# Optimization experiments

Hardware: AMD Instinct MI355X
Metric: run time of the kernel (lower is better)

## Reference

```python
import jax, jax.numpy as jnp
import numpy as np
from jax import lax

VOL, PATCH, DIM, DEPTH, HEADS, DIM_HEAD, MLP, CH, B = 64, 8, 768, 4, 12, 64, 3072, 1, 2
INNER = HEADS * DIM_HEAD
GS = VOL // PATCH              # 8 -> N = 512 tokens
EPS = 1e-5


def _sincos_1d(embed_dim, pos):
    omega = np.arange(embed_dim // 2, dtype=float) / (embed_dim / 2.0)
    omega = 1.0 / 10000 ** omega
    out = np.einsum('m,d->md', pos.reshape(-1), omega)
    return np.concatenate([np.sin(out), np.cos(out)], axis=1)


def _pos_embed_3d(embed_dim, gs):
    gd = np.arange(gs, dtype=np.float32)
    gh = np.arange(gs, dtype=np.float32)
    gw = np.arange(gs, dtype=np.float32)
    grid = np.stack(np.meshgrid(gw, gh, gd), axis=0).reshape([3, 1, gs, gs, gs])
    emb = np.concatenate([_sincos_1d(embed_dim // 3, grid[i]) for i in range(3)], axis=1)
    return jnp.asarray(emb, jnp.float32)[None]  # [1, N, dim]


def setup_inputs() -> dict:
    key = jax.random.key(0)
    ks = jax.random.split(key, 12)
    s = 0.02  # xavier-like small init scale
    d = {
        'volume': jax.random.normal(ks[0], (B, CH, VOL, VOL, VOL), jnp.float32),
        'conv_w': jax.random.normal(ks[1], (DIM, CH, PATCH, PATCH, PATCH), jnp.float32) * s,
        'conv_b': jnp.zeros((DIM,), jnp.float32),
        'pos_embed': _pos_embed_3d(DIM, GS),
        'ln1_w': jnp.ones((DEPTH, DIM), jnp.float32),
        'ln1_b': jnp.zeros((DEPTH, DIM), jnp.float32),
        'w_qkv': jax.random.normal(ks[2], (DEPTH, DIM, 3 * INNER), jnp.float32) * s,
        'w_o': jax.random.normal(ks[3], (DEPTH, INNER, DIM), jnp.float32) * s,
        'b_o': jnp.zeros((DEPTH, DIM), jnp.float32),
        'ln2_w': jnp.ones((DEPTH, DIM), jnp.float32),
        'ln2_b': jnp.zeros((DEPTH, DIM), jnp.float32),
        'w1': jax.random.normal(ks[4], (DEPTH, DIM, MLP), jnp.float32) * s,
        'b1': jnp.zeros((DEPTH, MLP), jnp.float32),
        'w2': jax.random.normal(ks[5], (DEPTH, MLP, DIM), jnp.float32) * s,
        'b2': jnp.zeros((DEPTH, DIM), jnp.float32),
        'lnf_w': jnp.ones((DIM,), jnp.float32),
        'lnf_b': jnp.zeros((DIM,), jnp.float32),
    }
    return d


def _ln(x, w, b):
    m = jnp.mean(x, axis=-1, keepdims=True)
    v = jnp.mean(jnp.square(x - m), axis=-1, keepdims=True)
    return (x - m) * lax.rsqrt(v + EPS) * w + b


def _forward(volume, conv_w, conv_b, pos_embed, ln1_w, ln1_b, w_qkv, w_o, b_o,
             ln2_w, ln2_b, w1, b1, w2, b2, lnf_w, lnf_b):
    # Conv3d patch embedding (stride == kernel == patch)
    x = lax.conv_general_dilated(volume, conv_w, window_strides=(PATCH,) * 3,
                                 padding='VALID',
                                 dimension_numbers=('NCDHW', 'OIDHW', 'NCDHW'))
    x = x + conv_b[None, :, None, None, None]
    b = x.shape[0]
    x = x.reshape(b, DIM, -1).transpose(0, 2, 1)   # b (d h w) c -> [B, N, dim]
    x = x + pos_embed
    scale = DIM_HEAD ** -0.5

    def layer(x, p):
        l1w, l1b, wqkv, wo, bo, l2w, l2b, W1, B1, W2, B2 = p
        h = _ln(x, l1w, l1b)
        qkv = h @ wqkv                               # [B, N, 3*inner]
        q, k, v = jnp.split(qkv, 3, axis=-1)
        def heads(t):
            bsz, n, _ = t.shape
            return t.reshape(bsz, n, HEADS, DIM_HEAD).transpose(0, 2, 1, 3)
        q, k, v = heads(q), heads(k), heads(v)
        attn = jax.nn.softmax(jnp.einsum('bhqd,bhkd->bhqk', q, k) * scale, axis=-1)
        o = jnp.einsum('bhqk,bhkd->bhqd', attn, v)   # [B, H, N, dh]
        o = o.transpose(0, 2, 1, 3).reshape(x.shape[0], -1, INNER)
        x = x + (o @ wo + bo)
        h = _ln(x, l2w, l2b)
        x = x + (jnp.tanh(h @ W1 + B1) @ W2 + B2)
        return x, None

    params = (ln1_w, ln1_b, w_qkv, w_o, b_o, ln2_w, ln2_b, w1, b1, w2, b2)
    x, _ = lax.scan(layer, x, params)
    return _ln(x, lnf_w, lnf_b)


def reference(volume, conv_w, conv_b, pos_embed, ln1_w, ln1_b, w_qkv, w_o, b_o,
              ln2_w, ln2_b, w1, b1, w2, b2, lnf_w, lnf_b):
    return _forward(volume, conv_w, conv_b, pos_embed, ln1_w, ln1_b, w_qkv, w_o, b_o,
                    ln2_w, ln2_b, w1, b1, w2, b2, lnf_w, lnf_b)
```

## Files before the change

### kernel.cpp

```cpp
#include <hip/hip_runtime.h>
#include <hip/hip_bf16.h>

typedef __hip_bfloat16 bf16;
typedef short bf16x8 __attribute__((ext_vector_type(8)));
typedef float f32x4 __attribute__((ext_vector_type(4)));

__device__ __forceinline__ float b2f(bf16 v) { return __bfloat162float(v); }
__device__ __forceinline__ void storev(float* p, float v) { *p = v; }
__device__ __forceinline__ void storev(bf16* p, float v) { *p = __float2bfloat16(v); }

__device__ __forceinline__ void gl2lds16(const bf16* g, bf16* l) {
  __builtin_amdgcn_global_load_lds(
      (const __attribute__((address_space(1))) unsigned int*)g,
      (__attribute__((address_space(3))) unsigned int*)l, 16, 0, 0);
}

__global__ void im2col_kernel(const float* __restrict__ vol, bf16* __restrict__ out) {
  int t = blockIdx.x;
  int b = t >> 9, n = t & 511;
  int pd = n >> 6, ph = (n >> 3) & 7, pw = n & 7;
  const float* vb = vol + ((size_t)b << 18);
  for (int l = threadIdx.x; l < 512; l += 256) {
    int i = l >> 6, j = (l >> 3) & 7, k = l & 7;
    out[(size_t)t * 512 + l] =
        __float2bfloat16(vb[(pd * 8 + i) * 4096 + (ph * 8 + j) * 64 + (pw * 8 + k)]);
  }
}

__global__ void convert_kernel(const float* __restrict__ in, bf16* __restrict__ out, int n) {
  int i = (blockIdx.x * 256 + threadIdx.x) * 4;
  if (i + 3 < n) {
    float4 v = *(const float4*)&in[i];
    out[i + 0] = __float2bfloat16(v.x);
    out[i + 1] = __float2bfloat16(v.y);
    out[i + 2] = __float2bfloat16(v.z);
    out[i + 3] = __float2bfloat16(v.w);
  }
}

__global__ __launch_bounds__(256) void transpose_all(
    const float* __restrict__ wqkv, const float* __restrict__ wo,
    const float* __restrict__ w1, const float* __restrict__ w2,
    bf16* __restrict__ tqkv, bf16* __restrict__ two,
    bf16* __restrict__ t1, bf16* __restrict__ t2) {
  int bid = blockIdx.x;
  size_t L = blockIdx.y;
  const float* in;
  bf16* out;
  int R, C, tc, t0;
  if (bid < 432)       { in = wqkv + L * 768 * 2304; out = tqkv + L * 768 * 2304; R = 768;  C = 2304; tc = 36; t0 = bid; }
  else if (bid < 576)  { in = wo + L * 768 * 768;    out = two + L * 768 * 768;   R = 768;  C = 768;  tc = 12; t0 = bid - 432; }
  else if (bid < 1152) { in = w1 + L * 768 * 3072;   out = t1 + L * 768 * 3072;   R = 768;  C = 3072; tc = 48; t0 = bid - 576; }
  else                 { in = w2 + L * 3072 * 768;   out = t2 + L * 3072 * 768;   R = 3072; C = 768;  tc = 12; t0 = bid - 1152; }
  int r0 = (t0 / tc) * 64, c0 = (t0 % tc) * 64;
  __shared__ bf16 Ts[64 * 68];
  int t = threadIdx.x;
  int r = t >> 4, cq = t & 15;
#pragma unroll
  for (int yy = 0; yy < 4; ++yy) {
    int row = r + yy * 16;
    float4 v = *(const float4*)&in[(size_t)(r0 + row) * C + c0 + cq * 4];
    bf16 pk[4] = {__float2bfloat16(v.x), __float2bfloat16(v.y),
                  __float2bfloat16(v.z), __float2bfloat16(v.w)};
    *(uint2*)&Ts[row * 68 + cq * 4] = *(uint2*)pk;
  }
  __syncthreads();
  int oc = t >> 2, seg = t & 3;
  bf16 pk[16];
#pragma unroll
  for (int j = 0; j < 16; ++j) {
    int e = (j + seg * 4) & 15;
    pk[e] = Ts[(seg * 16 + e) * 68 + oc];
  }
  *(uint4*)&out[(size_t)(c0 + oc) * R + r0 + seg * 16] = *(uint4*)&pk[0];
  *(uint4*)&out[(size_t)(c0 + oc) * R + r0 + seg * 16 + 8] = *(uint4*)&pk[8];
}

template <typename OutT>
__global__ __launch_bounds__(256) void ln_kernel(const float* __restrict__ x,
                                                 const float* __restrict__ w,
                                                 const float* __restrict__ b,
                                                 OutT* __restrict__ out) {
  int row = blockIdx.x * 4 + (threadIdx.x >> 6);
  int lane = threadIdx.x & 63;
  const float* xr = x + (size_t)row * 768;
  float v[12];
  float s = 0.f, ss = 0.f;
#pragma unroll
  for (int i = 0; i < 12; ++i) {
    v[i] = xr[lane + i * 64];
    s += v[i];
    ss += v[i] * v[i];
  }
  for (int off = 32; off; off >>= 1) {
    s += __shfl_xor(s, off);
    ss += __shfl_xor(ss, off);
  }
  float m = s * (1.f / 768.f);
  float var = ss * (1.f / 768.f) - m * m;
  float rr = rsqrtf(var + 1e-5f);
#pragma unroll
  for (int i = 0; i < 12; ++i)
    storev(out + (size_t)row * 768 + lane + i * 64,
           (v[i] - m) * rr * w[lane + i * 64] + b[lane + i * 64]);
}

template <int BM, int BN, int EPI>
__global__ __launch_bounds__(256) void mfma_gemm(
    const bf16* __restrict__ A, const bf16* __restrict__ Bt,
    const float* __restrict__ bias, const float* __restrict__ aux,
    bf16* __restrict__ vt,
    void* __restrict__ Cout, int M, int N, int K) {
  constexpr int WTM = BM / 2, WTN = BN / 2;
  constexpr int MT = WTM / 16, NT = WTN / 16;
  __shared__ bf16 As[BM * 64];
  __shared__ bf16 Bs[BN * 64];
  int tid = threadIdx.x;
  int wave = tid >> 6, lane = tid & 63;
  int wm = wave >> 1, wn = wave & 1;
  int m15 = lane & 15, q = lane >> 4;
  int m0 = blockIdx.y * BM, n0 = blockIdx.x * BN;
  int kspan = K / gridDim.z;
  int kbeg = blockIdx.z * kspan, kend = kbeg + kspan;

  f32x4 acc[MT][NT];
#pragma unroll
  for (int i = 0; i < MT; ++i)
#pragma unroll
    for (int j = 0; j < NT; ++j) acc[i][j] = (f32x4){0.f, 0.f, 0.f, 0.f};

  for (int k0 = kbeg; k0 < kend; k0 += 64) {
#pragma unroll
    for (int it = 0; it < BM * 8 / 256; ++it) {
      int c = tid + it * 256;
      int row = c >> 3, cc = c & 7;
      gl2lds16(&A[(size_t)(m0 + row) * K + k0 + cc * 8], &As[c * 8]);
    }
#pragma unroll
    for (int it = 0; it < BN * 8 / 256; ++it) {
      int c = tid + it * 256;
      int row = c >> 3, cc = c & 7;
      gl2lds16(&Bt[(size_t)(n0 + row) * K + k0 + cc * 8], &Bs[c * 8]);
    }
    __syncthreads();
#pragma unroll
    for (int s = 0; s < 2; ++s) {
      bf16x8 af[MT], bfr[NT];
#pragma unroll
      for (int i = 0; i < MT; ++i)
        af[i] = *(const bf16x8*)&As[(wm * WTM + i * 16 + m15) * 64 + s * 32 + q * 8];
#pragma unroll
      for (int j = 0; j < NT; ++j)
        bfr[j] = *(const bf16x8*)&Bs[(wn * WTN + j * 16 + m15) * 64 + s * 32 + q * 8];
#pragma unroll
      for (int i = 0; i < MT; ++i)
#pragma unroll
        for (int j = 0; j < NT; ++j)
          acc[i][j] = __builtin_amdgcn_mfma_f32_16x16x32_bf16(af[i], bfr[j], acc[i][j], 0, 0, 0);
    }
    __syncthreads();
  }

#pragma unroll
  for (int i = 0; i < MT; ++i) {
#pragma unroll
    for (int j = 0; j < NT; ++j) {
      int col = n0 + wn * WTN + j * 16 + m15;
      if (EPI == 4) {
        if (col < 1536) {
#pragma unroll
          for (int r = 0; r < 4; ++r) {
            int row = m0 + wm * WTM + i * 16 + q * 4 + r;
            ((bf16*)Cout)[(size_t)row * 1536 + col] = __float2bfloat16(acc[i][j][r]);
          }
        } else {
          int row0 = m0 + wm * WTM + i * 16 + q * 4;
          int cl = col - 1536;
          int hh = cl >> 6, dd = cl & 63;
          int bb = row0 >> 9, tok = row0 & 511;
          bf16 pk[4];
#pragma unroll
          for (int r = 0; r < 4; ++r) pk[r] = __float2bfloat16(acc[i][j][r]);
          *(uint2*)&vt[((size_t)(bb * 12 + hh) * 64 + dd) * 512 + tok] = *(uint2*)pk;
        }
      } else if (EPI == 5) {
        float bv = (blockIdx.z == 0) ? bias[col] : 0.f;
#pragma unroll
        for (int r = 0; r < 4; ++r) {
          int row = m0 + wm * WTM + i * 16 + q * 4 + r;
          unsafeAtomicAdd(&((float*)Cout)[(size_t)row * N + col], acc[i][j][r] + bv);
        }
      } else {
        float bv = (EPI == 0) ? 0.f : bias[col];
#pragma unroll
        for (int r = 0; r < 4; ++r) {
          int row = m0 + wm * WTM + i * 16 + q * 4 + r;
          float v = acc[i][j][r] + bv;
          if (EPI == 2) v = tanhf(v);
          if (EPI == 3) v += aux[(size_t)(row & 511) * N + col];
          if (EPI == 0 || EPI == 2)
            ((bf16*)Cout)[(size_t)row * N + col] = __float2bfloat16(v);
          else
            ((float*)Cout)[(size_t)row * N + col] = v;
        }
      }
    }
  }
}

__global__ __launch_bounds__(128) void attn_mfma(const bf16* __restrict__ qk,
                                                 const bf16* __restrict__ Vt,
                                                 bf16* __restrict__ o) {
  constexpr int PS = 520;
  __shared__ bf16 KVs[64 * 64];
  __shared__ bf16 P[32 * PS];
  int bh = blockIdx.x;
  int b = bh / 12, hh = bh % 12;
  int q0 = blockIdx.y * 32;
  int tid = threadIdx.x;
  int wave = tid >> 6, lane = tid & 63;
  int n15 = lane & 15, quad = lane >> 4;
  const bf16* qkb = qk + (size_t)b * 512 * 1536;
  int ql = wave * 16 + n15;

  const bf16* qp = qkb + (size_t)(q0 + ql) * 1536 + hh * 64 + quad * 8;
  bf16x8 qf0 = *(const bf16x8*)qp;
  bf16x8 qf1 = *(const bf16x8*)(qp + 32);

  f32x4 S[32];
#pragma unroll
  for (int i = 0; i < 32; ++i) S[i] = (f32x4){0.f, 0.f, 0.f, 0.f};

  const bf16* kbase = qkb + 768 + hh * 64;
#pragma unroll
  for (int kc = 0; kc < 8; ++kc) {
    __syncthreads();
#pragma unroll
    for (int it = 0; it < 4; ++it) {
      int c = tid + it * 128;
      int r = c >> 3, cc = c & 7;
      gl2lds16(&kbase[(size_t)(kc * 64 + r) * 1536 + cc * 8], &KVs[c * 8]);
    }
    __syncthreads();
#pragma unroll
    for (int t = 0; t < 4; ++t) {
      int idx = kc * 4 + t;
      bf16x8 a0 = *(const bf16x8*)&KVs[(t * 16 + n15) * 64 + quad * 8];
      bf16x8 a1 = *(const bf16x8*)&KVs[(t * 16 + n15) * 64 + 32 + quad * 8];
      S[idx] = __builtin_amdgcn_mfma_f32_16x16x32_bf16(a0, qf0, S[idx], 0, 0, 0);
      S[idx] = __builtin_amdgcn_mfma_f32_16x16x32_bf16(a1, qf1, S[idx], 0, 0, 0);
    }
  }

  float mx = -1e30f;
#pragma unroll
  for (int i = 0; i < 32; ++i)
#pragma unroll
    for (int r = 0; r < 4; ++r) { S[i][r] *= 0.125f; mx = fmaxf(mx, S[i][r]); }
  mx = fmaxf(mx, __shfl_xor(mx, 16));
  mx = fmaxf(mx, __shfl_xor(mx, 32));
  float sum = 0.f;
#pragma unroll
  for (int i = 0; i < 32; ++i)
#pragma unroll
    for (int r = 0; r < 4; ++r) { float e = __expf(S[i][r] - mx); S[i][r] = e; sum += e; }
  sum += __shfl_xor(sum, 16);
  sum += __shfl_xor(sum, 32);
  float inv = 1.f / sum;

#pragma unroll
  for (int i = 0; i < 32; ++i) {
    bf16 pk[4];
#pragma unroll
    for (int r = 0; r < 4; ++r) pk[r] = __float2bfloat16(S[i][r] * inv);
    *(uint2*)&P[(size_t)ql * PS + i * 16 + quad * 4] = *(uint2*)pk;
  }

  f32x4 oacc[4];
#pragma unroll
  for (int dt = 0; dt < 4; ++dt) oacc[dt] = (f32x4){0.f, 0.f, 0.f, 0.f};
  const bf16* vtb = Vt + (size_t)bh * 64 * 512;
  for (int kc = 0; kc < 8; ++kc) {
    __syncthreads();
#pragma unroll
    for (int it = 0; it < 4; ++it) {
      int c = tid + it * 128;
      int r = c >> 3, cc = c & 7;
      gl2lds16(&vtb[(size_t)r * 512 + kc * 64 + cc * 8], &KVs[c * 8]);
    }
    __syncthreads();
    bf16x8 p0 = *(const bf16x8*)&P[(size_t)ql * PS + kc * 64 + quad * 8];
    bf16x8 p1 = *(const bf16x8*)&P[(size_t)ql * PS + kc * 64 + 32 + quad * 8];
#pragma unroll
    for (int dt = 0; dt < 4; ++dt) {
      bf16x8 v0 = *(const bf16x8*)&KVs[(dt * 16 + n15) * 64 + quad * 8];
      bf16x8 v1 = *(const bf16x8*)&KVs[(dt * 16 + n15) * 64 + 32 + quad * 8];
      oacc[dt] = __builtin_amdgcn_mfma_f32_16x16x32_bf16(p0, v0, oacc[dt], 0, 0, 0);
      oacc[dt] = __builtin_amdgcn_mfma_f32_16x16x32_bf16(p1, v1, oacc[dt], 0, 0, 0);
    }
  }

#pragma unroll
  for (int dt = 0; dt < 4; ++dt)
#pragma unroll
    for (int r = 0; r < 4; ++r) {
      int tok = q0 + wave * 16 + quad * 4 + r;
      o[((size_t)b * 512 + tok) * 768 + hh * 64 + dt * 16 + n15] =
          __float2bfloat16(oacc[dt][r]);
    }
}

extern "C" void kernel_launch(void* const* d_in, const int* in_sizes, int n_in,
                              void* d_out, int out_size, void* d_ws, size_t ws_size,
                              hipStream_t stream) {
  const float* volume = (const float*)d_in[0];
  const float* conv_w = (const float*)d_in[1];
  const float* conv_b = (const float*)d_in[2];
  const float* pos    = (const float*)d_in[3];
  const float* ln1w   = (const float*)d_in[4];
  const float* ln1b   = (const float*)d_in[5];
  const float* wqkv   = (const float*)d_in[6];
  const float* wo     = (const float*)d_in[7];
  const float* bo     = (const float*)d_in[8];
  const float* ln2w   = (const float*)d_in[9];
  const float* ln2b   = (const float*)d_in[10];
  const float* w1     = (const float*)d_in[11];
  const float* b1     = (const float*)d_in[12];
  const float* w2     = (const float*)d_in[13];
  const float* b2     = (const float*)d_in[14];
  const float* lnfw   = (const float*)d_in[15];
  const float* lnfb   = (const float*)d_in[16];

  char* w = (char*)d_ws;
  float* x    = (float*)(w + 0);
  bf16* h     = (bf16*)(w + 3145728);
  bf16* qk    = (bf16*)(w + 4718592);
  bf16* patchA= qk;
  bf16* Vt    = (bf16*)(w + 7864320);
  bf16* oact  = (bf16*)(w + 9437184);
  bf16* cwb   = (bf16*)(w + 15728640);
  bf16* tqkv  = (bf16*)(w + 16515072);
  bf16* two   = (bf16*)(w + 30670848);
  bf16* t1    = (bf16*)(w + 35389440);
  bf16* t2    = (bf16*)(w + 54263808);

  convert_kernel<<<384, 256, 0, stream>>>(conv_w, cwb, 768 * 512);
  im2col_kernel<<<1024, 256, 0, stream>>>(volume, patchA);
  transpose_all<<<dim3(1728, 4), 256, 0, stream>>>(wqkv, wo, w1, w2, tqkv, two, t1, t2);
  mfma_gemm<64, 64, 3><<<dim3(12, 16), 256, 0, stream>>>(
      patchA, cwb, conv_b, pos, nullptr, x, 1024, 768, 512);

  for (int L = 0; L < 4; ++L) {
    ln_kernel<bf16><<<256, 256, 0, stream>>>(x, ln1w + L * 768, ln1b + L * 768, h);
    mfma_gemm<128, 64, 4><<<dim3(36, 8), 256, 0, stream>>>(
        h, tqkv + (size_t)L * 768 * 2304, nullptr, nullptr, Vt, qk, 1024, 2304, 768);
    attn_mfma<<<dim3(24, 16), 128, 0, stream>>>(qk, Vt, oact);
    mfma_gemm<64, 64, 5><<<dim3(12, 16, 2), 256, 0, stream>>>(
        oact, two + (size_t)L * 768 * 768, bo + L * 768, nullptr, nullptr, x, 1024, 768, 768);
    ln_kernel<bf16><<<256, 256, 0, stream>>>(x, ln2w + L * 768, ln2b + L * 768, h);
    mfma_gemm<128, 64, 2><<<dim3(48, 8), 256, 0, stream>>>(
        h, t1 + (size_t)L * 768 * 3072, b1 + L * 3072, nullptr, nullptr, oact, 1024, 3072, 768);
    mfma_gemm<64, 64, 5><<<dim3(12, 16, 4), 256, 0, stream>>>(
        oact, t2 + (size_t)L * 768 * 3072, b2 + L * 768, nullptr, nullptr, x, 1024, 768, 3072);
  }

  ln_kernel<float><<<256, 256, 0, stream>>>(x, lnfw, lnfb, (float*)d_out);
}
```

Before: 556.0 us.

## Split-K FC1 and patch GEMMs with atomics, shrink QKV tiles, rewrite transpose

FC1 now uses split-K (z=2) with atomic float accumulation into a zeroed fp32 buffer, followed by a separate bias+tanh kernel that writes bf16. The patch-embed GEMM also becomes split-K with atomics after a memset. The QKV GEMM switches to 64x64 tiles to launch more blocks. The weight-transpose kernel is rewritten to use an fp32 shared tile. The goal is more parallelism on a large GPU, paid for with memsets, atomic traffic, an extra fp32 round trip and an additional kernel launch.

```diff
diff --git a/kernel.cpp b/kernel.cpp
--- a/kernel.cpp
+++ b/kernel.cpp
@@ -53,27 +53,27 @@
   else if (bid < 1152) { in = w1 + L * 768 * 3072;   out = t1 + L * 768 * 3072;   R = 768;  C = 3072; tc = 48; t0 = bid - 576; }
   else                 { in = w2 + L * 3072 * 768;   out = t2 + L * 3072 * 768;   R = 3072; C = 768;  tc = 12; t0 = bid - 1152; }
   int r0 = (t0 / tc) * 64, c0 = (t0 % tc) * 64;
-  __shared__ bf16 Ts[64 * 68];
-  int t = threadIdx.x;
-  int r = t >> 4, cq = t & 15;
+  __shared__ float tile[64][65];
+  int tx = threadIdx.x & 15, ty = threadIdx.x >> 4;
 #pragma unroll
   for (int yy = 0; yy < 4; ++yy) {
-    int row = r + yy * 16;
-    float4 v = *(const float4*)&in[(size_t)(r0 + row) * C + c0 + cq * 4];
-    bf16 pk[4] = {__float2bfloat16(v.x), __float2bfloat16(v.y),
-                  __float2bfloat16(v.z), __float2bfloat16(v.w)};
-    *(uint2*)&Ts[row * 68 + cq * 4] = *(uint2*)pk;
+    float4 v = *(const float4*)&in[(size_t)(r0 + ty + yy * 16) * C + c0 + tx * 4];
+    tile[ty + yy * 16][tx * 4 + 0] = v.x;
+    tile[ty + yy * 16][tx * 4 + 1] = v.y;
+    tile[ty + yy * 16][tx * 4 + 2] = v.z;
+    tile[ty + yy * 16][tx * 4 + 3] = v.w;
   }
   __syncthreads();
-  int oc = t >> 2, seg = t & 3;
-  bf16 pk[16];
-#pragma unroll
-  for (int j = 0; j < 16; ++j) {
-    int e = (j + seg * 4) & 15;
-    pk[e] = Ts[(seg * 16 + e) * 68 + oc];
-  }
-  *(uint4*)&out[(size_t)(c0 + oc) * R + r0 + seg * 16] = *(uint4*)&pk[0];
-  *(uint4*)&out[(size_t)(c0 + oc) * R + r0 + seg * 16 + 8] = *(uint4*)&pk[8];
+  int cl = threadIdx.x >> 3;
+  int rb = (threadIdx.x & 7) * 8;
+#pragma unroll
+  for (int half = 0; half < 2; ++half) {
+    int c = cl + half * 32;
+    bf16 pk[8];
+#pragma unroll
+    for (int e = 0; e < 8; ++e) pk[e] = __float2bfloat16(tile[rb + e][c]);
+    *(uint4*)&out[(size_t)(c0 + c) * R + r0 + rb] = *(uint4*)pk;
+  }
 }
 
 template <typename OutT>
@@ -103,6 +103,25 @@
   for (int i = 0; i < 12; ++i)
     storev(out + (size_t)row * 768 + lane + i * 64,
            (v[i] - m) * rr * w[lane + i * 64] + b[lane + i * 64]);
+}
+
+__global__ __launch_bounds__(256) void act_kernel(const float* __restrict__ in,
+                                                  const float* __restrict__ b1,
+                                                  bf16* __restrict__ out) {
+  int row = blockIdx.x, tid = threadIdx.x;
+  const float* ir = in + (size_t)row * 3072;
+  bf16* orow = out + (size_t)row * 3072;
+#pragma unroll
+  for (int i = 0; i < 3; ++i) {
+    int c = tid * 4 + i * 1024;
+    float4 v = *(const float4*)&ir[c];
+    float4 bb = *(const float4*)&b1[c];
+    bf16 pk[4] = {__float2bfloat16(tanhf(v.x + bb.x)),
+                  __float2bfloat16(tanhf(v.y + bb.y)),
+                  __float2bfloat16(tanhf(v.z + bb.z)),
+                  __float2bfloat16(tanhf(v.w + bb.w))};
+    *(uint2*)&orow[c] = *(uint2*)pk;
+  }
 }
 
 template <int BM, int BN, int EPI>
@@ -190,6 +209,20 @@
           int row = m0 + wm * WTM + i * 16 + q * 4 + r;
           unsafeAtomicAdd(&((float*)Cout)[(size_t)row * N + col], acc[i][j][r] + bv);
         }
+      } else if (EPI == 6) {
+#pragma unroll
+        for (int r = 0; r < 4; ++r) {
+          int row = m0 + wm * WTM + i * 16 + q * 4 + r;
+          unsafeAtomicAdd(&((float*)Cout)[(size_t)row * N + col], acc[i][j][r]);
+        }
+      } else if (EPI == 7) {
+#pragma unroll
+        for (int r = 0; r < 4; ++r) {
+          int row = m0 + wm * WTM + i * 16 + q * 4 + r;
+          float v = acc[i][j][r];
+          if (blockIdx.z == 0) v += bias[col] + aux[(size_t)(row & 511) * N + col];
+          unsafeAtomicAdd(&((float*)Cout)[(size_t)row * N + col], v);
+        }
       } else {
         float bv = (EPI == 0) ? 0.f : bias[col];
 #pragma unroll
@@ -197,11 +230,7 @@
           int row = m0 + wm * WTM + i * 16 + q * 4 + r;
           float v = acc[i][j][r] + bv;
           if (EPI == 2) v = tanhf(v);
-          if (EPI == 3) v += aux[(size_t)(row & 511) * N + col];
-          if (EPI == 0 || EPI == 2)
-            ((bf16*)Cout)[(size_t)row * N + col] = __float2bfloat16(v);
-          else
-            ((float*)Cout)[(size_t)row * N + col] = v;
+          ((bf16*)Cout)[(size_t)row * N + col] = __float2bfloat16(v);
         }
       }
     }
@@ -343,23 +372,27 @@
   bf16* two   = (bf16*)(w + 30670848);
   bf16* t1    = (bf16*)(w + 35389440);
   bf16* t2    = (bf16*)(w + 54263808);
+  float* oactf= (float*)(w + 73138176);
 
   convert_kernel<<<384, 256, 0, stream>>>(conv_w, cwb, 768 * 512);
   im2col_kernel<<<1024, 256, 0, stream>>>(volume, patchA);
   transpose_all<<<dim3(1728, 4), 256, 0, stream>>>(wqkv, wo, w1, w2, tqkv, two, t1, t2);
-  mfma_gemm<64, 64, 3><<<dim3(12, 16), 256, 0, stream>>>(
+  hipMemsetAsync(x, 0, 1024 * 768 * sizeof(float), stream);
+  mfma_gemm<64, 64, 7><<<dim3(12, 16, 2), 256, 0, stream>>>(
       patchA, cwb, conv_b, pos, nullptr, x, 1024, 768, 512);
 
   for (int L = 0; L < 4; ++L) {
     ln_kernel<bf16><<<256, 256, 0, stream>>>(x, ln1w + L * 768, ln1b + L * 768, h);
-    mfma_gemm<128, 64, 4><<<dim3(36, 8), 256, 0, stream>>>(
+    mfma_gemm<64, 64, 4><<<dim3(36, 16), 256, 0, stream>>>(
         h, tqkv + (size_t)L * 768 * 2304, nullptr, nullptr, Vt, qk, 1024, 2304, 768);
     attn_mfma<<<dim3(24, 16), 128, 0, stream>>>(qk, Vt, oact);
     mfma_gemm<64, 64, 5><<<dim3(12, 16, 2), 256, 0, stream>>>(
         oact, two + (size_t)L * 768 * 768, bo + L * 768, nullptr, nullptr, x, 1024, 768, 768);
     ln_kernel<bf16><<<256, 256, 0, stream>>>(x, ln2w + L * 768, ln2b + L * 768, h);
-    mfma_gemm<128, 64, 2><<<dim3(48, 8), 256, 0, stream>>>(
-        h, t1 + (size_t)L * 768 * 3072, b1 + L * 3072, nullptr, nullptr, oact, 1024, 3072, 768);
+    hipMemsetAsync(oactf, 0, 1024 * 3072 * sizeof(float), stream);
+    mfma_gemm<64, 64, 6><<<dim3(48, 16, 2), 256, 0, stream>>>(
+        h, t1 + (size_t)L * 768 * 3072, nullptr, nullptr, nullptr, oactf, 1024, 3072, 768);
+    act_kernel<<<1024, 256, 0, stream>>>(oactf, b1 + L * 3072, oact);
     mfma_gemm<64, 64, 5><<<dim3(12, 16, 4), 256, 0, stream>>>(
         oact, t2 + (size_t)L * 768 * 3072, b2 + L * 768, nullptr, nullptr, x, 1024, 768, 3072);
   }
```

Result: slower. 594.6 us (+7.0%).
